# Kernel tuning notes

Measured on AMD Instinct MI355X. Metric: run time of the kernel, lower is better.

The kernel has to match this reference:

```python
import jax, jax.numpy as jnp
import numpy as np

T, D, H, HD = 4096, 1536, 12, 128  # tokens, hidden, heads, head_dim
NEG = -1e9


def rotate_half(x):
    x1, x2 = jnp.split(x, 2, axis=-1)
    return jnp.concatenate((-x2, x1), axis=-1)


def setup_inputs() -> dict:
    key = jax.random.key(0)
    k1, k2, k3, k4 = jax.random.split(key, 4)
    hidden_states = jax.random.normal(k1, (T, D), dtype=jnp.float32)
    cu_seqlens = (jnp.arange(5, dtype=jnp.int32) * (T // 4))  # [0,1024,2048,3072,4096]
    # rotary angles: positions within each segment times inverse frequencies
    pos = jnp.arange(T, dtype=jnp.float32) % (T // 4)
    inv_freq = 1.0 / (10000.0 ** (jnp.arange(0, HD // 2, dtype=jnp.float32) / (HD // 2)))
    rotary_pos_emb = pos[:, None] * inv_freq[None, :]  # (T, HD//2)
    w_qkv = jax.random.normal(k2, (3 * D, D), dtype=jnp.float32) * (D ** -0.5)
    w_proj = jax.random.normal(k3, (D, D), dtype=jnp.float32) * (D ** -0.5)
    return {"hidden_states": hidden_states, "cu_seqlens": cu_seqlens,
            "rotary_pos_emb": rotary_pos_emb, "w_qkv": w_qkv, "w_proj": w_proj}


def reference(hidden_states, cu_seqlens, rotary_pos_emb, w_qkv, w_proj):
    seq_len = hidden_states.shape[0]
    scaling = HD ** -0.5
    # fused QKV projection: (T, 3D) -> (3, T, H, HD)
    qkv = (hidden_states @ w_qkv.T).reshape(seq_len, 3, H, HD).transpose(1, 0, 2, 3)
    q, k, v = qkv[0], qkv[1], qkv[2]
    # RoPE (vision style): emb = cat(rpe, rpe) along last dim
    emb = jnp.concatenate((rotary_pos_emb, rotary_pos_emb), axis=-1)  # (T, HD)
    cos = jnp.cos(emb)[:, None, :]  # (T, 1, HD) broadcast over heads
    sin = jnp.sin(emb)[:, None, :]
    q = q * cos + rotate_half(q) * sin
    k = k * cos + rotate_half(k) * sin
    # block-diagonal mask from cu_seqlens (varlen packing)
    seg_id = jnp.searchsorted(cu_seqlens[1:], jnp.arange(seq_len), side="right")
    block_mask = seg_id[:, None] == seg_id[None, :]  # (T, T) bool
    # attention per head: (H, T, HD)
    qh = q.transpose(1, 0, 2)
    kh = k.transpose(1, 0, 2)
    vh = v.transpose(1, 0, 2)
    scores = jnp.einsum("htd,hsd->hts", qh, kh) * scaling
    scores = jnp.where(block_mask[None, :, :], scores, NEG)
    attn = jax.nn.softmax(scores, axis=-1)
    out = jnp.einsum("hts,hsd->htd", attn, vh)  # (H, T, HD)
    out = out.transpose(1, 0, 2).reshape(seq_len, D)
    return out @ w_proj.T


if __name__ == "__main__":
    o = reference(**setup_inputs())
    print(o.shape, o.dtype)
```

## Files before the change

### kernel.cpp

```cpp
#include <hip/hip_runtime.h>
#include <stdint.h>

#define TT 4096
#define DD 1536
#define NH 12
#define HD_ 128

typedef __bf16 bf16x8 __attribute__((ext_vector_type(8)));
typedef float  f32x4  __attribute__((ext_vector_type(4)));
typedef float  f32x16 __attribute__((ext_vector_type(16)));

__device__ __forceinline__ unsigned short f2b(float f) {
  union { float f; uint32_t u; } x; x.f = f;
  uint32_t r = x.u + 0x7fffu + ((x.u >> 16) & 1u);
  return (unsigned short)(r >> 16);
}
__device__ __forceinline__ float b2f(unsigned short b) {
  union { uint32_t u; float f; } x; x.u = ((uint32_t)b) << 16;
  return x.f;
}

__device__ __forceinline__ f32x16 mfma32(bf16x8 a, bf16x8 b, f32x16 c) {
  return __builtin_amdgcn_mfma_f32_32x32x16_bf16(a, b, c, 0, 0, 0);
}

__device__ __forceinline__ void async16(const void* g, void* l) {
  __builtin_amdgcn_global_load_lds((const __attribute__((address_space(1))) uint32_t*)g,
                                   (__attribute__((address_space(3))) uint32_t*)l,
                                   16, 0, 0);
}

__global__ void aux_kernel(const float* __restrict__ hs,
                           const float* __restrict__ wqkv,
                           const float* __restrict__ wproj,
                           const float* __restrict__ rpe,
                           unsigned short* __restrict__ hb,
                           unsigned short* __restrict__ wq,
                           unsigned short* __restrict__ wp,
                           float* __restrict__ cs, float* __restrict__ sn) {
  const int b = blockIdx.x;
  if (b < 15360) {
    const float* in;
    unsigned short* out;
    int base;
    if (b < 6144)       { in = hs;    out = hb; base = b; }
    else if (b < 13056) { in = wqkv;  out = wq; base = b - 6144; }
    else                { in = wproj; out = wp; base = b - 13056; }
    int i = (base * 256 + threadIdx.x) * 4;
    float4 v = *reinterpret_cast<const float4*>(in + i);
    ushort4 o;
    o.x = f2b(v.x); o.y = f2b(v.y); o.z = f2b(v.z); o.w = f2b(v.w);
    *reinterpret_cast<ushort4*>(out + i) = o;
  } else {
    int i = (b - 15360) * 256 + threadIdx.x;
    float e = rpe[i];
    float s, c;
    sincosf(e, &s, &c);
    cs[i] = c;
    sn[i] = s;
  }
}

__global__ __launch_bounds__(256, 4) void gemm_qkv_kernel(
    const unsigned short* __restrict__ A, const unsigned short* __restrict__ B,
    unsigned short* __restrict__ Qp, unsigned short* __restrict__ Kp,
    unsigned short* __restrict__ Vt, const float* __restrict__ csT,
    const float* __restrict__ snT) {
  __shared__ char smem[32768];
  const int tid = threadIdx.x;
  const int lane = tid & 63;
  const int wave = tid >> 6;
  const int wm = wave >> 1, wn = wave & 1;
  const int lr = lane & 15, lh = lane >> 4;

  const int m0 = blockIdx.x * 128;
  const int n0 = blockIdx.y * 128;

  const int srow = tid >> 2;
  const int schunk = (tid & 3) ^ (srow & 3);
  const unsigned short* Ag = A + (size_t)(m0 + srow) * DD + schunk * 8;
  const unsigned short* Bg = B + (size_t)(n0 + srow) * DD + schunk * 8;

#define STAGE_G(BUF, K0)                                            \
  {                                                                 \
    unsigned short* la = (unsigned short*)(smem + (BUF) * 16384);   \
    unsigned short* lb = la + 4096;                                 \
    async16(Ag + (K0), &la[tid * 8]);                               \
    async16(Ag + (K0) + (size_t)64 * DD, &la[2048 + tid * 8]);      \
    async16(Bg + (K0), &lb[tid * 8]);                               \
    async16(Bg + (K0) + (size_t)64 * DD, &lb[2048 + tid * 8]);      \
  }

  const int csw = (lr & 3);
  f32x4 acc[4][4] = {};
  STAGE_G(0, 0);
  __syncthreads();
  int cur = 0;
  for (int k0 = 0; k0 < DD; k0 += 32) {
    const int kn = (k0 + 32 < DD) ? (k0 + 32) : k0;
    STAGE_G(cur ^ 1, kn);
    const unsigned short* la = (const unsigned short*)(smem + cur * 16384);
    const unsigned short* lb = la + 4096;
    bf16x8 af[4], bfr[4];
#pragma unroll
    for (int i = 0; i < 4; i++) {
      af[i]  = *reinterpret_cast<const bf16x8*>(
          &la[(wm * 64 + i * 16 + lr) * 32 + (lh ^ csw) * 8]);
      bfr[i] = *reinterpret_cast<const bf16x8*>(
          &lb[(i * 32 + wn * 16 + lr) * 32 + (lh ^ csw) * 8]);
    }
#pragma unroll
    for (int i = 0; i < 4; i++)
#pragma unroll
      for (int j = 0; j < 4; j++)
        acc[i][j] = __builtin_amdgcn_mfma_f32_16x16x32_bf16(af[i], bfr[j], acc[i][j], 0, 0, 0);
    __syncthreads();
    cur ^= 1;
  }
#undef STAGE_G

  const int s  = n0 / DD;
  const int hh = (n0 - s * DD) >> 7;

  if (s == 2) {
#pragma unroll
    for (int i = 0; i < 4; i++)
#pragma unroll
      for (int j = 0; j < 4; j++) {
        const int dd = j * 32 + wn * 16 + lr;
        const int t0 = m0 + wm * 64 + i * 16 + lh * 4;
        ushort4 st;
        st.x = f2b(acc[i][j][0]); st.y = f2b(acc[i][j][1]);
        st.z = f2b(acc[i][j][2]); st.w = f2b(acc[i][j][3]);
        *reinterpret_cast<ushort4*>(&Vt[((size_t)(hh * HD_ + dd)) * TT + t0]) = st;
      }
  } else {
    unsigned short* dst = (s == 0) ? Qp : Kp;
    const float scale =
        (s == 0) ? (0.08838834764831845f * 1.4426950408889634f) : 1.0f;
#pragma unroll
    for (int i = 0; i < 4; i++) {
#pragma unroll
      for (int j = 0; j < 4; j++) {
        const int dd = j * 32 + wn * 16 + lr;
        const int d2 = dd & 63;
        const float sgn = (dd < 64) ? -1.f : 1.f;
#pragma unroll
        for (int r = 0; r < 4; r++) {
          const int t = m0 + wm * 64 + i * 16 + lh * 4 + r;
          const float own = acc[i][j][r];
          const float par = acc[i][j ^ 2][r];
          const float c   = csT[t * 64 + d2];
          const float sn_ = snT[t * 64 + d2];
          dst[((size_t)hh * TT + t) * HD_ + dd] =
              f2b((own * c + sgn * par * sn_) * scale);
        }
        __builtin_amdgcn_sched_barrier(0);
      }
    }
  }
}

__global__ __launch_bounds__(512) void attn_kernel(
    const unsigned short* __restrict__ Qp, const unsigned short* __restrict__ Kp,
    const unsigned short* __restrict__ Vt, const int* __restrict__ cu,
    unsigned short* __restrict__ AO) {
  __shared__ unsigned short lds[32768];
  const int bid = blockIdx.x;
  const int tid = threadIdx.x;
  const int wave = tid >> 6;
  const int lane = tid & 63;
  const int lq = lane & 31;
  const int hi = lane >> 5;
  const int swz = lq & 7;

  const int xcd  = bid & 7;
  const int idx  = bid >> 3;
  const int pair = xcd * 6 + (idx >> 2);
  const int qblk = idx & 3;
  const int h    = pair >> 2;
  const int seg  = pair & 3;
  const int kstart = cu[seg], kend = cu[seg + 1];
  const int q0 = kstart + (qblk * 8 + wave) * 32;

  const unsigned short* Kh = Kp + (size_t)h * TT * HD_;
  const unsigned short* Vh = Vt + (size_t)h * HD_ * TT;

  const int krow0 = tid >> 4, kc0 = tid & 15;
  const int vrow0 = tid >> 3, vc0 = tid & 7;

#define STAGE_TILE(BUF, KT)                                                    \
  {                                                                            \
    unsigned short* Lk = &lds[(BUF) * 16384];                                  \
    unsigned short* Lv = Lk + 8192;                                            \
    _Pragma("unroll")                                                          \
    for (int r = 0; r < 2; r++) {                                              \
      int row = krow0 + r * 32;                                                \
      int c = kc0 ^ (row & 7);                                                 \
      async16(Kh + (size_t)((KT) + row) * HD_ + c * 8, Lk + tid * 8 + r * 4096); \
    }                                                                          \
    _Pragma("unroll")                                                          \
    for (int r = 0; r < 2; r++) {                                              \
      int row = vrow0 + r * 64;                                                \
      int c = vc0 ^ (row & 7);                                                 \
      async16(Vh + (size_t)row * TT + (KT) + c * 8, Lv + tid * 8 + r * 4096);  \
    }                                                                          \
  }

  const unsigned short* Qg = Qp + ((size_t)h * TT + q0 + lq) * HD_ + hi * 8;
  bf16x8 qf[8];
#pragma unroll
  for (int s = 0; s < 8; s++)
    qf[s] = *reinterpret_cast<const bf16x8*>(Qg + s * 16);

  STAGE_TILE(0, kstart);
  __syncthreads();

  f32x16 o0 = {}, o1 = {}, o2 = {}, o3 = {};
  float lsum = 0.f;
  int cur = 0;

  for (int kt = kstart; kt < kend; kt += 64) {
    const int ktn = (kt + 64 < kend) ? (kt + 64) : kt;
    STAGE_TILE(cur ^ 1, ktn);

    const unsigned short* Kl = &lds[cur * 16384];
    const unsigned short* Vl = Kl + 8192;

    f32x16 sA = {}, sB = {};
#pragma unroll
    for (int s = 0; s < 8; s++) {
      bf16x8 kf = *reinterpret_cast<const bf16x8*>(
          Kl + lq * 128 + (((s << 1) | hi) ^ swz) * 8);
      sA = mfma32(kf, qf[s], sA);
    }
#pragma unroll
    for (int s = 0; s < 8; s++) {
      bf16x8 kf = *reinterpret_cast<const bf16x8*>(
          Kl + 4096 + lq * 128 + (((s << 1) | hi) ^ swz) * 8);
      sB = mfma32(kf, qf[s], sB);
    }

    bf16x8 pfrag[4];
    float acc0 = 0.f, acc1 = 0.f;
#pragma unroll
    for (int g = 0; g < 4; g++) {
      const f32x16 S = (g & 2) ? sB : sA;
      const int b = (g & 1) * 8;
      float e0 = __builtin_amdgcn_exp2f(S[b + 0]);
      float e1 = __builtin_amdgcn_exp2f(S[b + 1]);
      float e2 = __builtin_amdgcn_exp2f(S[b + 2]);
      float e3 = __builtin_amdgcn_exp2f(S[b + 3]);
      float e4 = __builtin_amdgcn_exp2f(S[b + 4]);
      float e5 = __builtin_amdgcn_exp2f(S[b + 5]);
      float e6 = __builtin_amdgcn_exp2f(S[b + 6]);
      float e7 = __builtin_amdgcn_exp2f(S[b + 7]);
      acc0 += (e0 + e1) + (e2 + e3);
      acc1 += (e4 + e5) + (e6 + e7);
      union PW { uint32_t u; __bf16 e[2]; } p0, p1, p2, p3;
      p0.e[0] = (__bf16)e0; p0.e[1] = (__bf16)e1;
      p1.e[0] = (__bf16)e2; p1.e[1] = (__bf16)e3;
      p2.e[0] = (__bf16)e4; p2.e[1] = (__bf16)e5;
      p3.e[0] = (__bf16)e6; p3.e[1] = (__bf16)e7;
      uint32_t W2 = (uint32_t)__shfl_xor((int)(hi ? p0.u : p2.u), 32);
      uint32_t W3 = (uint32_t)__shfl_xor((int)(hi ? p1.u : p3.u), 32);
      union F { uint32_t w[4]; bf16x8 v; } f;
      f.w[0] = hi ? W2 : p0.u;
      f.w[1] = hi ? W3 : p1.u;
      f.w[2] = hi ? p2.u : W2;
      f.w[3] = hi ? p3.u : W3;
      pfrag[g] = f.v;
    }
    float tsum = acc0 + acc1;
    lsum += tsum + __shfl_xor(tsum, 32);

#pragma unroll
    for (int g = 0; g < 4; g++) {
      const int co = (((g << 1) | hi) ^ swz) * 8;
      bf16x8 v0 = *reinterpret_cast<const bf16x8*>(Vl + (lq)       * 64 + co);
      bf16x8 v1 = *reinterpret_cast<const bf16x8*>(Vl + (32 + lq)  * 64 + co);
      bf16x8 v2 = *reinterpret_cast<const bf16x8*>(Vl + (64 + lq)  * 64 + co);
      bf16x8 v3 = *reinterpret_cast<const bf16x8*>(Vl + (96 + lq)  * 64 + co);
      o0 = mfma32(v0, pfrag[g], o0);
      o1 = mfma32(v1, pfrag[g], o1);
      o2 = mfma32(v2, pfrag[g], o2);
      o3 = mfma32(v3, pfrag[g], o3);
    }

    __syncthreads();
    cur ^= 1;
  }
#undef STAGE_TILE

  const float inv = 1.0f / lsum;
  unsigned short* Ab = AO + (size_t)(q0 + lq) * DD + h * HD_ + 4 * hi;
#pragma unroll
  for (int dblk = 0; dblk < 4; dblk++) {
    f32x16 o = (dblk == 0) ? o0 : (dblk == 1) ? o1 : (dblk == 2) ? o2 : o3;
#pragma unroll
    for (int rq = 0; rq < 4; rq++) {
      ushort4 st;
      st.x = f2b(o[rq * 4 + 0] * inv);
      st.y = f2b(o[rq * 4 + 1] * inv);
      st.z = f2b(o[rq * 4 + 2] * inv);
      st.w = f2b(o[rq * 4 + 3] * inv);
      *reinterpret_cast<ushort4*>(Ab + dblk * 32 + rq * 8) = st;
    }
  }
}

__global__ __launch_bounds__(256, 4) void gemm_out_kernel(
    const unsigned short* __restrict__ A, const unsigned short* __restrict__ B,
    float* __restrict__ C) {
  __shared__ char smem[32768];
  const int tid = threadIdx.x;
  const int lane = tid & 63;
  const int wave = tid >> 6;
  const int wm = wave >> 1, wn = wave & 1;
  const int lr = lane & 15, lh = lane >> 4;
  const int m0 = blockIdx.x * 128, n0 = blockIdx.y * 128;

  const int srow = tid >> 2;
  const int schunk = (tid & 3) ^ (srow & 3);
  const unsigned short* Ag = A + (size_t)(m0 + srow) * DD + schunk * 8;
  const unsigned short* Bg = B + (size_t)(n0 + srow) * DD + schunk * 8;

#define STAGE_G(BUF, K0)                                            \
  {                                                                 \
    unsigned short* la = (unsigned short*)(smem + (BUF) * 16384);   \
    unsigned short* lb = la + 4096;                                 \
    async16(Ag + (K0), &la[tid * 8]);                               \
    async16(Ag + (K0) + (size_t)64 * DD, &la[2048 + tid * 8]);      \
    async16(Bg + (K0), &lb[tid * 8]);                               \
    async16(Bg + (K0) + (size_t)64 * DD, &lb[2048 + tid * 8]);      \
  }

  const int csw = (lr & 3);
  f32x4 acc[4][4] = {};
  STAGE_G(0, 0);
  __syncthreads();
  int cur = 0;
  for (int k0 = 0; k0 < DD; k0 += 32) {
    const int kn = (k0 + 32 < DD) ? (k0 + 32) : k0;
    STAGE_G(cur ^ 1, kn);
    const unsigned short* la = (const unsigned short*)(smem + cur * 16384);
    const unsigned short* lb = la + 4096;
    bf16x8 af[4], bfr[4];
#pragma unroll
    for (int i = 0; i < 4; i++) {
      af[i]  = *reinterpret_cast<const bf16x8*>(
          &la[(wm * 64 + i * 16 + lr) * 32 + (lh ^ csw) * 8]);
      bfr[i] = *reinterpret_cast<const bf16x8*>(
          &lb[(wn * 64 + i * 16 + lr) * 32 + (lh ^ csw) * 8]);
    }
#pragma unroll
    for (int i = 0; i < 4; i++)
#pragma unroll
      for (int j = 0; j < 4; j++)
        acc[i][j] = __builtin_amdgcn_mfma_f32_16x16x32_bf16(af[i], bfr[j], acc[i][j], 0, 0, 0);
    __syncthreads();
    cur ^= 1;
  }
#undef STAGE_G

#pragma unroll
  for (int i = 0; i < 4; i++)
#pragma unroll
    for (int j = 0; j < 4; j++) {
      int cn = n0 + wn * 64 + j * 16 + lr;
#pragma unroll
      for (int r = 0; r < 4; r++) {
        int t = m0 + wm * 64 + i * 16 + lh * 4 + r;
        C[(size_t)t * DD + cn] = acc[i][j][r];
      }
    }
}

extern "C" void kernel_launch(void* const* d_in, const int* in_sizes, int n_in,
                              void* d_out, int out_size, void* d_ws, size_t ws_size,
                              hipStream_t stream) {
  const float* hs    = (const float*)d_in[0];
  const int*   cu    = (const int*)d_in[1];
  const float* rpe   = (const float*)d_in[2];
  const float* wqkv  = (const float*)d_in[3];
  const float* wproj = (const float*)d_in[4];
  float* out = (float*)d_out;
  char* ws = (char*)d_ws;

  unsigned short* hb = (unsigned short*)(ws + 0);
  unsigned short* wq = (unsigned short*)(ws + 12582912);
  unsigned short* wp = (unsigned short*)(ws + 26738688);
  unsigned short* Qp = (unsigned short*)(ws + 31457280);
  unsigned short* Kp = (unsigned short*)(ws + 44040192);
  unsigned short* Vt = (unsigned short*)(ws + 56623104);

  float* csT = out;
  float* snT = csT + TT * 64;

  aux_kernel<<<16384, 256, 0, stream>>>(hs, wqkv, wproj, rpe, hb, wq, wp, csT, snT);

  gemm_qkv_kernel<<<dim3(32, 36), 256, 0, stream>>>(hb, wq, Qp, Kp, Vt, csT, snT);

  attn_kernel<<<192, 512, 0, stream>>>(Qp, Kp, Vt, cu, hb );

  gemm_out_kernel<<<dim3(32, 12), 256, 0, stream>>>(hb , wp, out);
}
```

Before: 167.1 us.

## Widen QKV GEMM tile to 128x256 with 8 waves and drop LDS swizzle

The QKV projection GEMM now uses 512-thread blocks that each compute a 128x256 output tile covering two heads, which halves the grid in N and reuses each staged A tile across twice as many columns. The epilogue indexing is remapped so each wave pair writes its own head, keeping the RoPE partner columns within one wave. The XOR chunk swizzle on LDS loads is removed in both GEMMs, simplifying addressing at the risk of more LDS bank conflicts. LDS use per block grows to 48KB, and the larger block may reduce occupancy.

```diff
diff --git a/kernel.cpp b/kernel.cpp
--- a/kernel.cpp
+++ b/kernel.cpp
@@ -61,37 +61,33 @@
   }
 }
 
-__global__ __launch_bounds__(256, 4) void gemm_qkv_kernel(
+__global__ __launch_bounds__(512, 4) void gemm_qkv_kernel(
     const unsigned short* __restrict__ A, const unsigned short* __restrict__ B,
     unsigned short* __restrict__ Qp, unsigned short* __restrict__ Kp,
     unsigned short* __restrict__ Vt, const float* __restrict__ csT,
     const float* __restrict__ snT) {
-  __shared__ char smem[32768];
+  __shared__ char smem[49152];
   const int tid = threadIdx.x;
   const int lane = tid & 63;
-  const int wave = tid >> 6;
-  const int wm = wave >> 1, wn = wave & 1;
+  const int wid = tid >> 6;
+  const int wm = wid >> 2, wn = wid & 3;
   const int lr = lane & 15, lh = lane >> 4;
 
   const int m0 = blockIdx.x * 128;
-  const int n0 = blockIdx.y * 128;
-
-  const int srow = tid >> 2;
-  const int schunk = (tid & 3) ^ (srow & 3);
-  const unsigned short* Ag = A + (size_t)(m0 + srow) * DD + schunk * 8;
-  const unsigned short* Bg = B + (size_t)(n0 + srow) * DD + schunk * 8;
-
-#define STAGE_G(BUF, K0)                                            \
-  {                                                                 \
-    unsigned short* la = (unsigned short*)(smem + (BUF) * 16384);   \
-    unsigned short* lb = la + 4096;                                 \
-    async16(Ag + (K0), &la[tid * 8]);                               \
-    async16(Ag + (K0) + (size_t)64 * DD, &la[2048 + tid * 8]);      \
-    async16(Bg + (K0), &lb[tid * 8]);                               \
-    async16(Bg + (K0) + (size_t)64 * DD, &lb[2048 + tid * 8]);      \
-  }
-
-  const int csw = (lr & 3);
+  const int n0 = blockIdx.y * 256;
+
+  const unsigned short* Ag = A + (size_t)(m0 + (tid >> 2)) * DD + (tid & 3) * 8;
+  const unsigned short* Bg = B + (size_t)(n0 + (tid >> 2)) * DD + (tid & 3) * 8;
+
+#define STAGE_G(BUF, K0)                                             \
+  {                                                                  \
+    unsigned short* la = (unsigned short*)(smem + (BUF) * 24576);    \
+    unsigned short* lb = la + 4096;                                  \
+    async16(Ag + (K0), &la[tid * 8]);                                \
+    async16(Bg + (K0), &lb[tid * 8]);                                \
+    async16(Bg + (K0) + (size_t)128 * DD, &lb[4096 + tid * 8]);      \
+  }
+
   f32x4 acc[4][4] = {};
   STAGE_G(0, 0);
   __syncthreads();
@@ -99,15 +95,18 @@
   for (int k0 = 0; k0 < DD; k0 += 32) {
     const int kn = (k0 + 32 < DD) ? (k0 + 32) : k0;
     STAGE_G(cur ^ 1, kn);
-    const unsigned short* la = (const unsigned short*)(smem + cur * 16384);
+    const unsigned short* la = (const unsigned short*)(smem + cur * 24576);
     const unsigned short* lb = la + 4096;
     bf16x8 af[4], bfr[4];
 #pragma unroll
-    for (int i = 0; i < 4; i++) {
-      af[i]  = *reinterpret_cast<const bf16x8*>(
-          &la[(wm * 64 + i * 16 + lr) * 32 + (lh ^ csw) * 8]);
-      bfr[i] = *reinterpret_cast<const bf16x8*>(
-          &lb[(i * 32 + wn * 16 + lr) * 32 + (lh ^ csw) * 8]);
+    for (int i = 0; i < 4; i++)
+      af[i] = *reinterpret_cast<const bf16x8*>(
+          &la[(wm * 64 + i * 16 + lr) * 32 + lh * 8]);
+#pragma unroll
+    for (int j = 0; j < 4; j++) {
+      const int nrow = (wn >> 1) * 128 + (j >> 1) * 64 + (wn & 1) * 32 + (j & 1) * 16;
+      bfr[j] = *reinterpret_cast<const bf16x8*>(
+          &lb[(nrow + lr) * 32 + lh * 8]);
     }
 #pragma unroll
     for (int i = 0; i < 4; i++)
@@ -119,15 +118,16 @@
   }
 #undef STAGE_G
 
-  const int s  = n0 / DD;
-  const int hh = (n0 - s * DD) >> 7;
+  const int s   = n0 / DD;
+  const int rem = n0 - s * DD;
+  const int hh  = (rem >> 7) + (wn >> 1);
 
   if (s == 2) {
 #pragma unroll
     for (int i = 0; i < 4; i++)
 #pragma unroll
       for (int j = 0; j < 4; j++) {
-        const int dd = j * 32 + wn * 16 + lr;
+        const int dd = (j >> 1) * 64 + (wn & 1) * 32 + (j & 1) * 16 + lr;
         const int t0 = m0 + wm * 64 + i * 16 + lh * 4;
         ushort4 st;
         st.x = f2b(acc[i][j][0]); st.y = f2b(acc[i][j][1]);
@@ -142,7 +142,7 @@
     for (int i = 0; i < 4; i++) {
 #pragma unroll
       for (int j = 0; j < 4; j++) {
-        const int dd = j * 32 + wn * 16 + lr;
+        const int dd = (j >> 1) * 64 + (wn & 1) * 32 + (j & 1) * 16 + lr;
         const int d2 = dd & 63;
         const float sgn = (dd < 64) ? -1.f : 1.f;
 #pragma unroll
@@ -320,10 +320,8 @@
   const int lr = lane & 15, lh = lane >> 4;
   const int m0 = blockIdx.x * 128, n0 = blockIdx.y * 128;
 
-  const int srow = tid >> 2;
-  const int schunk = (tid & 3) ^ (srow & 3);
-  const unsigned short* Ag = A + (size_t)(m0 + srow) * DD + schunk * 8;
-  const unsigned short* Bg = B + (size_t)(n0 + srow) * DD + schunk * 8;
+  const unsigned short* Ag = A + (size_t)(m0 + (tid >> 2)) * DD + (tid & 3) * 8;
+  const unsigned short* Bg = B + (size_t)(n0 + (tid >> 2)) * DD + (tid & 3) * 8;
 
 #define STAGE_G(BUF, K0)                                            \
   {                                                                 \
@@ -335,7 +333,6 @@
     async16(Bg + (K0) + (size_t)64 * DD, &lb[2048 + tid * 8]);      \
   }
 
-  const int csw = (lr & 3);
   f32x4 acc[4][4] = {};
   STAGE_G(0, 0);
   __syncthreads();
@@ -348,10 +345,8 @@
     bf16x8 af[4], bfr[4];
 #pragma unroll
     for (int i = 0; i < 4; i++) {
-      af[i]  = *reinterpret_cast<const bf16x8*>(
-          &la[(wm * 64 + i * 16 + lr) * 32 + (lh ^ csw) * 8]);
-      bfr[i] = *reinterpret_cast<const bf16x8*>(
-          &lb[(wn * 64 + i * 16 + lr) * 32 + (lh ^ csw) * 8]);
+      af[i]  = *reinterpret_cast<const bf16x8*>(&la[(wm * 64 + i * 16 + lr) * 32 + lh * 8]);
+      bfr[i] = *reinterpret_cast<const bf16x8*>(&lb[(wn * 64 + i * 16 + lr) * 32 + lh * 8]);
     }
 #pragma unroll
     for (int i = 0; i < 4; i++)
@@ -399,7 +394,7 @@
 
   aux_kernel<<<16384, 256, 0, stream>>>(hs, wqkv, wproj, rpe, hb, wq, wp, csT, snT);
 
-  gemm_qkv_kernel<<<dim3(32, 36), 256, 0, stream>>>(hb, wq, Qp, Kp, Vt, csT, snT);
+  gemm_qkv_kernel<<<dim3(32, 18), 512, 0, stream>>>(hb, wq, Qp, Kp, Vt, csT, snT);
 
   attn_kernel<<<192, 512, 0, stream>>>(Qp, Kp, Vt, cu, hb );
 
```

Result: no change. 170.0 us (+1.7%).
